# Kernel optimization log

Hardware: AMD Instinct MI355X
Metric: run time of the kernel (lower is better)

The kernel has to match this reference:

```python
import jax, jax.numpy as jnp
import numpy as np

N_STU, N_ITEM, N_CONC = 10000, 50000, 2048
EDGES, K = 250000, 4
EMB, CNUM = 64, 128


def setup_inputs() -> dict:
    key = jax.random.key(0)
    ks = jax.random.split(key, 10)
    return {
        "stu_idx": jax.random.randint(ks[0], (EDGES,), 0, N_STU),
        "item_idx": jax.random.randint(ks[1], (EDGES,), 0, N_ITEM),
        "conc_idx": jax.random.randint(ks[2], (EDGES, K), 0, N_CONC),
        "stu_fusion": jax.random.normal(ks[3], (N_STU, EMB), jnp.float32),
        "item_fusion": jax.random.normal(ks[4], (N_ITEM, EMB), jnp.float32),
        "concept_fusion": jax.random.normal(ks[5], (N_CONC, EMB), jnp.float32),
        # factor weights are non-negative in the original (NoneNegClipper)
        "W_stu": jax.random.uniform(ks[6], (CNUM, 2 * EMB), jnp.float32) * 0.1,
        "W_item": jax.random.uniform(ks[7], (CNUM, 2 * EMB), jnp.float32) * 0.1,
        "w_pred": jax.random.uniform(ks[8], (CNUM,), jnp.float32) * 0.1,
        "b_pred": jax.random.normal(ks[9], (1,), jnp.float32),
    }


def reference(stu_idx, item_idx, conc_idx, stu_fusion, item_fusion,
              concept_fusion, W_stu, W_item, w_pred, b_pred):
    emb = stu_fusion.shape[1]
    # split Linear(2*emb -> CNUM) into the two cat halves: out = x1 @ Wa.T + x2 @ Wb.T
    Ws_a, Ws_b = W_stu[:, :emb], W_stu[:, emb:]
    Wi_a, Wi_b = W_item[:, :emb], W_item[:, emb:]

    # per-entity projections computed once on the tables, then gathered (cheap)
    stu_part = (stu_fusion @ Ws_a.T)[stu_idx]      # [E, CNUM]
    item_part = (item_fusion @ Wi_a.T)[item_idx]   # [E, CNUM]
    conc_stu = (concept_fusion @ Ws_b.T)[conc_idx]   # [E, K, CNUM]
    conc_item = (concept_fusion @ Wi_b.T)[conc_idx]  # [E, K, CNUM]

    stu_out = jax.nn.sigmoid(stu_part[:, None, :] + conc_stu)    # [E, K, CNUM]
    item_out = jax.nn.sigmoid(item_part[:, None, :] + conc_item)  # [E, K, CNUM]
    diff = stu_out - item_out
    per_conc = jax.nn.sigmoid(jnp.einsum('ekc,c->ek', diff, w_pred) + b_pred[0])  # [E, K]
    return per_conc.mean(axis=1)  # [E]
```

## Files before the change

### kernel.cpp

```cpp
#include <hip/hip_runtime.h>
#include <hip/hip_bf16.h>
#include <hip/hip_fp16.h>

constexpr int EDGES = 250000;
constexpr int EMB   = 64;
constexpr int CNUM  = 128;
constexpr int NSTU  = 10000;
constexpr int NITEM = 50000;
constexpr int NCONC = 2048;

constexpr size_t ESP_OFF = 0;
constexpr size_t EIP_OFF = ESP_OFF + (size_t)NSTU  * CNUM;
constexpr size_t ECS_OFF = EIP_OFF + (size_t)NITEM * CNUM;
constexpr size_t ECI_OFF = ECS_OFF + (size_t)NCONC * CNUM;

constexpr float NEG_LOG2E = -1.44269504088896340736f;

constexpr int STU_JOBS  = NSTU  / 16;
constexpr int ITEM_JOBS = NITEM / 16;
constexpr int CONC_JOBS = (NCONC / 16) * 2;
constexpr int NJOBS     = STU_JOBS + ITEM_JOBS + CONC_JOBS;
constexpr int PROJ_BLKS = (NJOBS + 3) / 4;

typedef _Float16 half8 __attribute__((ext_vector_type(8)));
typedef float    f32x4 __attribute__((ext_vector_type(4)));

__device__ __forceinline__ half8 pack8(float4 lo, float4 hi) {
    half8 h;
    h[0] = (_Float16)lo.x; h[1] = (_Float16)lo.y;
    h[2] = (_Float16)lo.z; h[3] = (_Float16)lo.w;
    h[4] = (_Float16)hi.x; h[5] = (_Float16)hi.y;
    h[6] = (_Float16)hi.z; h[7] = (_Float16)hi.w;
    return h;
}

__global__ __launch_bounds__(256) void proj_mfma(
        const float* __restrict__ stuF, const float* __restrict__ itemF,
        const float* __restrict__ concF,
        const float* __restrict__ W_stu, const float* __restrict__ W_item,
        __half* __restrict__ ESP, __half* __restrict__ EIP,
        __half* __restrict__ ECS, __half* __restrict__ ECI) {
    const int tid  = threadIdx.x;
    const int lane = tid & 63;
    const int job  = blockIdx.x * 4 + (tid >> 6);
    if (job >= NJOBS) return;

    const float* F; const float* W; __half* O; int strip, wcol;
    if (job < STU_JOBS) {
        F = stuF;  W = W_stu;  O = ESP; strip = job; wcol = 0;
    } else if (job < STU_JOBS + ITEM_JOBS) {
        F = itemF; W = W_item; O = EIP; strip = job - STU_JOBS; wcol = 0;
    } else {
        const int g = job - STU_JOBS - ITEM_JOBS;
        F = concF; W = (g & 1) ? W_item : W_stu; O = (g & 1) ? ECI : ECS;
        strip = g >> 1; wcol = EMB;
    }

    const int m = lane & 15;
    const int q = lane >> 4;
    const int row = strip * 16 + m;

    const float4* fa = (const float4*)(F + (size_t)row * EMB + q * 8);
    const float4* fb = (const float4*)(F + (size_t)row * EMB + 32 + q * 8);
    const half8 A0 = pack8(fa[0], fa[1]);
    const half8 A1 = pack8(fb[0], fb[1]);

    const int orow = strip * 16 + q * 4;

#pragma unroll
    for (int ct = 0; ct < 8; ++ct) {
        const int ch = ct * 16 + m;
        const float* wr = W + (size_t)ch * (2 * EMB) + wcol;
        const float4* wb0 = (const float4*)(wr + q * 8);
        const float4* wb1 = (const float4*)(wr + 32 + q * 8);
        const half8 B0 = pack8(wb0[0], wb0[1]);
        const half8 B1 = pack8(wb1[0], wb1[1]);

        f32x4 acc = {0.f, 0.f, 0.f, 0.f};
        acc = __builtin_amdgcn_mfma_f32_16x16x32_f16(A0, B0, acc, 0, 0, 0);
        acc = __builtin_amdgcn_mfma_f32_16x16x32_f16(A1, B1, acc, 0, 0, 0);

#pragma unroll
        for (int r = 0; r < 4; ++r) {
            const float e = __builtin_amdgcn_exp2f(acc[r] * NEG_LOG2E);
            O[(size_t)(orow + r) * CNUM + ct * 16 + m] = __float2half(e);
        }
    }
}

__device__ __forceinline__ void h8f(const uint4 u, float* f) {
    const __half2* h = (const __half2*)&u;
#pragma unroll
    for (int i = 0; i < 4; ++i) {
        float2 v = __half22float2(h[i]);
        f[2*i] = v.x; f[2*i+1] = v.y;
    }
}

__device__ __forceinline__ float chan(float es, float ec, float ei, float ecc,
                                      float w) {
    const float t = es * ec;
    const float u = ei * ecc;
    return (w * (u - t)) * __builtin_amdgcn_rcpf((1.f + t) * (1.f + u));
}

__device__ __forceinline__ float sigm(float x) {
    return __builtin_amdgcn_rcpf(1.f + __builtin_amdgcn_exp2f(x * NEG_LOG2E));
}

__global__ __launch_bounds__(256) void edge_kernel(
        const int*  __restrict__ stu_idx,
        const int*  __restrict__ item_idx,
        const int4* __restrict__ conc_idx,
        const __half* __restrict__ ESP,
        const __half* __restrict__ EIP,
        const __half* __restrict__ ECS,
        const __half* __restrict__ ECI,
        const float* __restrict__ w_pred,
        const float* __restrict__ b_pred,
        float* __restrict__ out) {
    const int lane = threadIdx.x & 63;
    const int wvg  = (blockIdx.x * blockDim.x + threadIdx.x) >> 6;
    const int sub  = lane >> 4;
    const int li   = lane & 15;
    const int e    = wvg * 4 + sub;

    const int s  = stu_idx[e];
    const int it = item_idx[e];
    const int4 c4 = conc_idx[e];

    float es[8], ei[8], wf[8];
    h8f(*(const uint4*)(ESP + (size_t)s  * CNUM + li * 8), es);
    h8f(*(const uint4*)(EIP + (size_t)it * CNUM + li * 8), ei);
    {
        const float4* wp4 = (const float4*)(w_pred + li * 8);
        float4 a = wp4[0], b4 = wp4[1];
        wf[0]=a.x; wf[1]=a.y; wf[2]=a.z; wf[3]=a.w;
        wf[4]=b4.x; wf[5]=b4.y; wf[6]=b4.z; wf[7]=b4.w;
    }
    const float b = b_pred[0];

    const int ck[4] = {c4.x, c4.y, c4.z, c4.w};
    float p[4];
#pragma unroll
    for (int k = 0; k < 4; ++k) {
        float cs[8], ci[8];
        h8f(*(const uint4*)(ECS + (size_t)ck[k] * CNUM + li * 8), cs);
        h8f(*(const uint4*)(ECI + (size_t)ck[k] * CNUM + li * 8), ci);
        float a0 = 0.f, a1 = 0.f;
#pragma unroll
        for (int j = 0; j < 8; j += 2) {
            a0 += chan(es[j],   cs[j],   ei[j],   ci[j],   wf[j]);
            a1 += chan(es[j+1], cs[j+1], ei[j+1], ci[j+1], wf[j+1]);
        }
        p[k] = a0 + a1;
    }

#pragma unroll
    for (int m = 1; m <= 8; m <<= 1) {
        p[0] += __shfl_xor(p[0], m, 64);
        p[1] += __shfl_xor(p[1], m, 64);
        p[2] += __shfl_xor(p[2], m, 64);
        p[3] += __shfl_xor(p[3], m, 64);
    }

    const float r = 0.25f * (sigm(p[0] + b) + sigm(p[1] + b) +
                             sigm(p[2] + b) + sigm(p[3] + b));
    if (li == 0) out[e] = r;
}

extern "C" void kernel_launch(void* const* d_in, const int* in_sizes, int n_in,
                              void* d_out, int out_size, void* d_ws, size_t ws_size,
                              hipStream_t stream) {
    const int* stu_idx  = (const int*)d_in[0];
    const int* item_idx = (const int*)d_in[1];
    const int* conc_idx = (const int*)d_in[2];
    const float* stu_fusion     = (const float*)d_in[3];
    const float* item_fusion    = (const float*)d_in[4];
    const float* concept_fusion = (const float*)d_in[5];
    const float* W_stu          = (const float*)d_in[6];
    const float* W_item         = (const float*)d_in[7];
    const float* w_pred         = (const float*)d_in[8];
    const float* b_pred         = (const float*)d_in[9];
    float* out = (float*)d_out;

    __half* ESP = (__half*)d_ws + ESP_OFF;
    __half* EIP = (__half*)d_ws + EIP_OFF;
    __half* ECS = (__half*)d_ws + ECS_OFF;
    __half* ECI = (__half*)d_ws + ECI_OFF;

    proj_mfma<<<PROJ_BLKS, 256, 0, stream>>>(
        stu_fusion, item_fusion, concept_fusion, W_stu, W_item,
        ESP, EIP, ECS, ECI);

    edge_kernel<<<EDGES / 16, 256, 0, stream>>>(
        stu_idx, item_idx, (const int4*)conc_idx,
        ESP, EIP, ECS, ECI, w_pred, b_pred, out);
}
```

Measured before the change: 145.2 us.

## Compute edge channel math in packed fp16 and reduce with DPP adds

The edge kernel now keeps the gathered fp16 projections packed and does the per-channel product, denominator, reciprocal and partial sums in half-precision vector arithmetic instead of converting to fp32. w_pred is pre-converted to fp16 in the projection kernel. The cross-lane reduction switches from shfl_xor to DPP row operations. This is meant to cut ALU and conversion instruction count in the edge kernel. The trade-off is lower accuracy, since fp16 reciprocal and fp16 accumulation can lose precision or overflow when t and u are large.

```diff
diff --git a/kernel.cpp b/kernel.cpp
--- a/kernel.cpp
+++ b/kernel.cpp
@@ -13,6 +13,7 @@
 constexpr size_t EIP_OFF = ESP_OFF + (size_t)NSTU  * CNUM;
 constexpr size_t ECS_OFF = EIP_OFF + (size_t)NITEM * CNUM;
 constexpr size_t ECI_OFF = ECS_OFF + (size_t)NCONC * CNUM;
+constexpr size_t WH_OFF  = ECI_OFF + (size_t)NCONC * CNUM;
 
 constexpr float NEG_LOG2E = -1.44269504088896340736f;
 
@@ -22,11 +23,13 @@
 constexpr int NJOBS     = STU_JOBS + ITEM_JOBS + CONC_JOBS;
 constexpr int PROJ_BLKS = (NJOBS + 3) / 4;
 
-typedef _Float16 half8 __attribute__((ext_vector_type(8)));
+typedef _Float16 h8 __attribute__((ext_vector_type(8)));
+typedef _Float16 h4 __attribute__((ext_vector_type(4)));
+typedef _Float16 h2 __attribute__((ext_vector_type(2)));
 typedef float    f32x4 __attribute__((ext_vector_type(4)));
 
-__device__ __forceinline__ half8 pack8(float4 lo, float4 hi) {
-    half8 h;
+__device__ __forceinline__ h8 pack8(float4 lo, float4 hi) {
+    h8 h;
     h[0] = (_Float16)lo.x; h[1] = (_Float16)lo.y;
     h[2] = (_Float16)lo.z; h[3] = (_Float16)lo.w;
     h[4] = (_Float16)hi.x; h[5] = (_Float16)hi.y;
@@ -34,18 +37,40 @@
     return h;
 }
 
+__device__ __forceinline__ _Float16 rcp16(_Float16 x) {
+#if __has_builtin(__builtin_amdgcn_rcph)
+    return __builtin_amdgcn_rcph(x);
+#else
+    return (_Float16)__builtin_amdgcn_rcpf((float)x);
+#endif
+}
+
+template <int CTRL>
+__device__ __forceinline__ float dppadd(float x) {
+    return x + __int_as_float(__builtin_amdgcn_update_dpp(
+        0, __float_as_int(x), CTRL, 0xf, 0xf, true));
+}
+
 __global__ __launch_bounds__(256) void proj_mfma(
         const float* __restrict__ stuF, const float* __restrict__ itemF,
         const float* __restrict__ concF,
         const float* __restrict__ W_stu, const float* __restrict__ W_item,
-        __half* __restrict__ ESP, __half* __restrict__ EIP,
-        __half* __restrict__ ECS, __half* __restrict__ ECI) {
+        const float* __restrict__ w_pred,
+        _Float16* __restrict__ ESP, _Float16* __restrict__ EIP,
+        _Float16* __restrict__ ECS, _Float16* __restrict__ ECI,
+        _Float16* __restrict__ WH) {
     const int tid  = threadIdx.x;
     const int lane = tid & 63;
     const int job  = blockIdx.x * 4 + (tid >> 6);
     if (job >= NJOBS) return;
 
-    const float* F; const float* W; __half* O; int strip, wcol;
+    if (job == 0) {
+        const float2 wv2 = ((const float2*)w_pred)[lane];
+        h2 wh; wh[0] = (_Float16)wv2.x; wh[1] = (_Float16)wv2.y;
+        *(h2*)(WH + 2 * lane) = wh;
+    }
+
+    const float* F; const float* W; _Float16* O; int strip, wcol;
     if (job < STU_JOBS) {
         F = stuF;  W = W_stu;  O = ESP; strip = job; wcol = 0;
     } else if (job < STU_JOBS + ITEM_JOBS) {
@@ -62,8 +87,8 @@
 
     const float4* fa = (const float4*)(F + (size_t)row * EMB + q * 8);
     const float4* fb = (const float4*)(F + (size_t)row * EMB + 32 + q * 8);
-    const half8 A0 = pack8(fa[0], fa[1]);
-    const half8 A1 = pack8(fb[0], fb[1]);
+    const h8 A0 = pack8(fa[0], fa[1]);
+    const h8 A1 = pack8(fb[0], fb[1]);
 
     const int orow = strip * 16 + q * 4;
 
@@ -73,8 +98,8 @@
         const float* wr = W + (size_t)ch * (2 * EMB) + wcol;
         const float4* wb0 = (const float4*)(wr + q * 8);
         const float4* wb1 = (const float4*)(wr + 32 + q * 8);
-        const half8 B0 = pack8(wb0[0], wb0[1]);
-        const half8 B1 = pack8(wb1[0], wb1[1]);
+        const h8 B0 = pack8(wb0[0], wb0[1]);
+        const h8 B1 = pack8(wb1[0], wb1[1]);
 
         f32x4 acc = {0.f, 0.f, 0.f, 0.f};
         acc = __builtin_amdgcn_mfma_f32_16x16x32_f16(A0, B0, acc, 0, 0, 0);
@@ -83,25 +108,9 @@
 #pragma unroll
         for (int r = 0; r < 4; ++r) {
             const float e = __builtin_amdgcn_exp2f(acc[r] * NEG_LOG2E);
-            O[(size_t)(orow + r) * CNUM + ct * 16 + m] = __float2half(e);
+            O[(size_t)(orow + r) * CNUM + ct * 16 + m] = (_Float16)e;
         }
     }
-}
-
-__device__ __forceinline__ void h8f(const uint4 u, float* f) {
-    const __half2* h = (const __half2*)&u;
-#pragma unroll
-    for (int i = 0; i < 4; ++i) {
-        float2 v = __half22float2(h[i]);
-        f[2*i] = v.x; f[2*i+1] = v.y;
-    }
-}
-
-__device__ __forceinline__ float chan(float es, float ec, float ei, float ecc,
-                                      float w) {
-    const float t = es * ec;
-    const float u = ei * ecc;
-    return (w * (u - t)) * __builtin_amdgcn_rcpf((1.f + t) * (1.f + u));
 }
 
 __device__ __forceinline__ float sigm(float x) {
@@ -112,11 +121,11 @@
         const int*  __restrict__ stu_idx,
         const int*  __restrict__ item_idx,
         const int4* __restrict__ conc_idx,
-        const __half* __restrict__ ESP,
-        const __half* __restrict__ EIP,
-        const __half* __restrict__ ECS,
-        const __half* __restrict__ ECI,
-        const float* __restrict__ w_pred,
+        const _Float16* __restrict__ ESP,
+        const _Float16* __restrict__ EIP,
+        const _Float16* __restrict__ ECS,
+        const _Float16* __restrict__ ECI,
+        const _Float16* __restrict__ WH,
         const float* __restrict__ b_pred,
         float* __restrict__ out) {
     const int lane = threadIdx.x & 63;
@@ -129,40 +138,42 @@
     const int it = item_idx[e];
     const int4 c4 = conc_idx[e];
 
-    float es[8], ei[8], wf[8];
-    h8f(*(const uint4*)(ESP + (size_t)s  * CNUM + li * 8), es);
-    h8f(*(const uint4*)(EIP + (size_t)it * CNUM + li * 8), ei);
-    {
-        const float4* wp4 = (const float4*)(w_pred + li * 8);
-        float4 a = wp4[0], b4 = wp4[1];
-        wf[0]=a.x; wf[1]=a.y; wf[2]=a.z; wf[3]=a.w;
-        wf[4]=b4.x; wf[5]=b4.y; wf[6]=b4.z; wf[7]=b4.w;
-    }
+    const h8 es = *(const h8*)(ESP + (size_t)s  * CNUM + li * 8);
+    const h8 ei = *(const h8*)(EIP + (size_t)it * CNUM + li * 8);
+    const h8 w8 = *(const h8*)(WH + li * 8);
     const float b = b_pred[0];
+
+    const h8 ONE = {(_Float16)1, (_Float16)1, (_Float16)1, (_Float16)1,
+                    (_Float16)1, (_Float16)1, (_Float16)1, (_Float16)1};
 
     const int ck[4] = {c4.x, c4.y, c4.z, c4.w};
     float p[4];
 #pragma unroll
     for (int k = 0; k < 4; ++k) {
-        float cs[8], ci[8];
-        h8f(*(const uint4*)(ECS + (size_t)ck[k] * CNUM + li * 8), cs);
-        h8f(*(const uint4*)(ECI + (size_t)ck[k] * CNUM + li * 8), ci);
-        float a0 = 0.f, a1 = 0.f;
-#pragma unroll
-        for (int j = 0; j < 8; j += 2) {
-            a0 += chan(es[j],   cs[j],   ei[j],   ci[j],   wf[j]);
-            a1 += chan(es[j+1], cs[j+1], ei[j+1], ci[j+1], wf[j+1]);
-        }
-        p[k] = a0 + a1;
-    }
-
-#pragma unroll
-    for (int m = 1; m <= 8; m <<= 1) {
-        p[0] += __shfl_xor(p[0], m, 64);
-        p[1] += __shfl_xor(p[1], m, 64);
-        p[2] += __shfl_xor(p[2], m, 64);
-        p[3] += __shfl_xor(p[3], m, 64);
-    }
+        const h8 cs = *(const h8*)(ECS + (size_t)ck[k] * CNUM + li * 8);
+        const h8 ci = *(const h8*)(ECI + (size_t)ck[k] * CNUM + li * 8);
+        const h8 t   = es * cs;
+        const h8 u   = ei * ci;
+        const h8 den = (t + ONE) * (u + ONE);
+        const h8 num = w8 * (u - t);
+        h8 r;
+#pragma unroll
+        for (int i = 0; i < 8; ++i) r[i] = num[i] * rcp16(den[i]);
+        const h4 q4 = __builtin_shufflevector(r, r, 0, 1, 2, 3)
+                    + __builtin_shufflevector(r, r, 4, 5, 6, 7);
+        const h2 q2 = __builtin_shufflevector(q4, q4, 0, 1)
+                    + __builtin_shufflevector(q4, q4, 2, 3);
+        p[k] = (float)q2[0] + (float)q2[1];
+    }
+
+#pragma unroll
+    for (int j = 0; j < 4; ++j) p[j] = dppadd<0xB1>(p[j]);
+#pragma unroll
+    for (int j = 0; j < 4; ++j) p[j] = dppadd<0x4E>(p[j]);
+#pragma unroll
+    for (int j = 0; j < 4; ++j) p[j] = dppadd<0x141>(p[j]);
+#pragma unroll
+    for (int j = 0; j < 4; ++j) p[j] = dppadd<0x140>(p[j]);
 
     const float r = 0.25f * (sigm(p[0] + b) + sigm(p[1] + b) +
                              sigm(p[2] + b) + sigm(p[3] + b));
@@ -184,16 +195,17 @@
     const float* b_pred         = (const float*)d_in[9];
     float* out = (float*)d_out;
 
-    __half* ESP = (__half*)d_ws + ESP_OFF;
-    __half* EIP = (__half*)d_ws + EIP_OFF;
-    __half* ECS = (__half*)d_ws + ECS_OFF;
-    __half* ECI = (__half*)d_ws + ECI_OFF;
+    _Float16* ESP = (_Float16*)d_ws + ESP_OFF;
+    _Float16* EIP = (_Float16*)d_ws + EIP_OFF;
+    _Float16* ECS = (_Float16*)d_ws + ECS_OFF;
+    _Float16* ECI = (_Float16*)d_ws + ECI_OFF;
+    _Float16* WH  = (_Float16*)d_ws + WH_OFF;
 
     proj_mfma<<<PROJ_BLKS, 256, 0, stream>>>(
-        stu_fusion, item_fusion, concept_fusion, W_stu, W_item,
-        ESP, EIP, ECS, ECI);
+        stu_fusion, item_fusion, concept_fusion, W_stu, W_item, w_pred,
+        ESP, EIP, ECS, ECI, WH);
 
     edge_kernel<<<EDGES / 16, 256, 0, stream>>>(
         stu_idx, item_idx, (const int4*)conc_idx,
-        ESP, EIP, ECS, ECI, w_pred, b_pred, out);
-}
+        ESP, EIP, ECS, ECI, WH, b_pred, out);
+}
```

After: 136.2 us. 6.2% less time.
